# Performance work log

Hardware: AMD Instinct MI355X
Metric: run time of the kernel (lower is better)

The kernel has to match this reference:

```python
import jax, jax.numpy as jnp
import numpy as np

TOP_K = 32

def setup_inputs() -> dict:
    key = jax.random.key(0)
    x = jax.random.normal(key, (4096, 32768), dtype=jnp.float32)
    return {"x": x}

def reference(x) -> jnp.ndarray:
    bsz, d_sae = x.shape
    k = min(TOP_K, d_sae)
    # top-k indices per row (unsorted order does not matter for masking)
    _, idxs = jax.lax.top_k(x, k)  # [batch, k]
    rows = jnp.arange(bsz)[:, None]  # [batch, 1]
    mask = jnp.zeros_like(x).at[rows, idxs].set(1.0)
    return mask * x
```

## Files before the change

kernel.cpp:

```cpp
#include <hip/hip_runtime.h>

#define TOPK    32
#define ROW     32768
#define THREADS 512
#define WAVES   8
#define VPT     16
#define BINS    2048
#define CAP     2048

__device__ __forceinline__ unsigned int f2key(float f) {
    unsigned int u = __float_as_uint(f);
    return u ^ (0x80000000u | (unsigned int)((int)u >> 31));
}
__device__ __forceinline__ float key2f(unsigned int k) {
    unsigned int u = (k & 0x80000000u) ? (k & 0x7fffffffu) : ~k;
    return __uint_as_float(u);
}

struct Shared {
    unsigned int hist[BINS];
    unsigned int wsum[WAVES];
    unsigned int sel_g, sel_gabove;
    unsigned int sel_bin, sel_above;
    unsigned int cand_cnt;
    unsigned int cnt_s;
    float        cf[CAP];
    unsigned int cidx[CAP];
};

__device__ __forceinline__ void hist_select(Shared& sh, int t, int lane,
                                            int wave, unsigned int kk) {
    const int base = wave * 256 + lane * 4;
    unsigned int h0 = sh.hist[base + 0], h1 = sh.hist[base + 1];
    unsigned int h2 = sh.hist[base + 2], h3 = sh.hist[base + 3];
    unsigned int p = h0 + h1 + h2 + h3;
    unsigned int s = p;
#pragma unroll
    for (int off = 1; off < 64; off <<= 1) {
        unsigned int vv = __shfl_down(s, off);
        if (lane + off < 64) s += vv;
    }
    if (lane == 0) sh.wsum[wave] = s;
    __syncthreads();

    if (t == 0) {
        unsigned int above = 0; int g = WAVES - 1;
        for (int w = WAVES - 1; w >= 0; --w) {
            if (above + sh.wsum[w] >= kk) { g = w; break; }
            above += sh.wsum[w];
        }
        sh.sel_g = (unsigned int)g; sh.sel_gabove = above;
    }
    __syncthreads();

    if (wave == (int)sh.sel_g) {
        unsigned int a = sh.sel_gabove + (s - p);
        unsigned int hh[4] = {h0, h1, h2, h3};
#pragma unroll
        for (int j = 3; j >= 0; --j) {
            unsigned int h = hh[j];
            if (a < kk && a + h >= kk) {
                sh.sel_bin = (unsigned int)(base + j);
                sh.sel_above = a;
            }
            a += h;
        }
    }
    __syncthreads();
}

__global__ __launch_bounds__(THREADS, 4) void topk_scatter_kernel(
    const float* __restrict__ x, float* __restrict__ out) {

    __shared__ Shared sh;
    const int row  = blockIdx.x;
    const int t    = threadIdx.x;
    const int lane = t & 63;
    const int wave = t >> 6;

    const float4* __restrict__ xin =
        reinterpret_cast<const float4*>(x + (size_t)row * ROW);
    float* __restrict__ orow = out + (size_t)row * ROW;

    float4 v[VPT];
#pragma unroll
    for (int i = 0; i < VPT; ++i) v[i] = xin[i * THREADS + t];

#pragma unroll
    for (int b = 0; b < 4; ++b) sh.hist[t + b * THREADS] = 0;
    if (t == 0) sh.cand_cnt = 0;
    __syncthreads();

    float m = -__builtin_inff();
#pragma unroll
    for (int i = 0; i < VPT; ++i)
        m = fmaxf(m, fmaxf(fmaxf(v[i].x, v[i].y), fmaxf(v[i].z, v[i].w)));

    atomicAdd(&sh.hist[f2key(m) >> 21], 1u);
    __syncthreads();

    hist_select(sh, t, lane, wave, TOPK);

    const float L = key2f(sh.sel_bin << 21);

#pragma unroll
    for (int i = 0; i < VPT; ++i) {
#pragma unroll
        for (int j = 0; j < 4; ++j) {
            float f = (&v[i].x)[j];
            if (f >= L) {
                unsigned int pos = atomicAdd(&sh.cand_cnt, 1u);
                if (pos < CAP) {
                    sh.cf[pos]   = f;
                    sh.cidx[pos] = (unsigned int)((i * THREADS + t) * 4 + j);
                }
            }
        }
    }
    __syncthreads();
    const unsigned int C = sh.cand_cnt;

    if (C <= CAP) {
        for (unsigned int i = t; i < C; i += THREADS) {
            float ki = sh.cf[i]; unsigned int ii = sh.cidx[i];
            unsigned int r = 0;
            for (unsigned int j = 0; j < C; ++j) {
                float kj = sh.cf[j];
                unsigned int ij = sh.cidx[j];
                r += (kj > ki || (kj == ki && ij < ii)) ? 1u : 0u;
            }
            if (r < TOPK) orow[ii] = ki;
        }
        return;
    }

    unsigned int prefix = 0; int pbits = 0;
    unsigned int kk = TOPK, e = 0;
    for (int r = 0; r < 3; ++r) {
        const int shift = (r == 0) ? 21 : (r == 1 ? 10 : 0);
        const int bits  = (r == 2) ? 10 : 11;
        const unsigned int msk = (1u << bits) - 1u;
        __syncthreads();
#pragma unroll
        for (int b = 0; b < 4; ++b) sh.hist[t + b * THREADS] = 0;
        __syncthreads();
#pragma unroll
        for (int i = 0; i < VPT; ++i) {
#pragma unroll
            for (int j = 0; j < 4; ++j) {
                unsigned int key = f2key((&v[i].x)[j]);
                bool match = (pbits == 0) || ((key >> (32 - pbits)) == prefix);
                if (match) atomicAdd(&sh.hist[(key >> shift) & msk], 1u);
            }
        }
        __syncthreads();
        hist_select(sh, t, lane, wave, kk);
        kk = kk - sh.sel_above;
        e  = sh.hist[sh.sel_bin];
        prefix = (prefix << bits) | sh.sel_bin;
        pbits += bits;
    }
    const unsigned int T = prefix;

    unsigned int Cc = ROW;
    if (e != kk) {
        unsigned int lo = 0, hi = ROW;
        while (hi - lo > 1u) {
            unsigned int mid = (lo + hi) >> 1;
            __syncthreads();
            if (t == 0) sh.cnt_s = 0;
            __syncthreads();
            unsigned int c = 0;
#pragma unroll
            for (int i = 0; i < VPT; ++i) {
#pragma unroll
                for (int j = 0; j < 4; ++j) {
                    unsigned int key = f2key((&v[i].x)[j]);
                    unsigned int idx = (unsigned int)((i * THREADS + t) * 4 + j);
                    if (key == T && idx < mid) ++c;
                }
            }
            if (c) atomicAdd(&sh.cnt_s, c);
            __syncthreads();
            if (sh.cnt_s >= kk) hi = mid; else lo = mid;
        }
        Cc = hi;
    }

#pragma unroll
    for (int i = 0; i < VPT; ++i) {
#pragma unroll
        for (int j = 0; j < 4; ++j) {
            float f = (&v[i].x)[j];
            unsigned int key = f2key(f);
            unsigned int idx = (unsigned int)((i * THREADS + t) * 4 + j);
            if (key > T || (key == T && idx < Cc)) orow[idx] = f;
        }
    }
}

extern "C" void kernel_launch(void* const* d_in, const int* in_sizes, int n_in,
                              void* d_out, int out_size, void* d_ws, size_t ws_size,
                              hipStream_t stream) {
    const float* x = (const float*)d_in[0];
    float* out = (float*)d_out;
    const int rows = in_sizes[0] / ROW;
    hipMemsetAsync(out, 0, (size_t)out_size * sizeof(float), stream);
    topk_scatter_kernel<<<rows, THREADS, 0, stream>>>(x, out);
}
```

Before: 239.4 us.

## Replace memset plus scatter with two-pass dense write, drop register row cache

Removes the separate hipMemsetAsync and instead writes the full output row densely inside the kernel. During the candidate pass every element at or above the threshold is written and everything else is zeroed, then rejected candidates are cleared afterwards. The block shrinks to 256 threads and no longer holds the row in registers; it re-reads x from global memory (likely L2 hits) on each pass, which should allow higher occupancy. The risk is the extra reads of x, plus a serial single-thread bin scan on the rare fallback path.

New measurement: 340.7 us. 1.42x slower.

```diff
diff --git a/kernel.cpp b/kernel.cpp
--- a/kernel.cpp
+++ b/kernel.cpp
@@ -2,11 +2,11 @@
 
 #define TOPK    32
 #define ROW     32768
-#define THREADS 512
-#define WAVES   8
-#define VPT     16
+#define THREADS 256
+#define WAVES   4
+#define F4PT    32
 #define BINS    2048
-#define CAP     2048
+#define CAP     1024
 
 __device__ __forceinline__ unsigned int f2key(float f) {
     unsigned int u = __float_as_uint(f);
@@ -30,10 +30,11 @@
 
 __device__ __forceinline__ void hist_select(Shared& sh, int t, int lane,
                                             int wave, unsigned int kk) {
-    const int base = wave * 256 + lane * 4;
-    unsigned int h0 = sh.hist[base + 0], h1 = sh.hist[base + 1];
-    unsigned int h2 = sh.hist[base + 2], h3 = sh.hist[base + 3];
-    unsigned int p = h0 + h1 + h2 + h3;
+    const int base = wave * 512 + lane * 8;
+    unsigned int h[8];
+    unsigned int p = 0;
+#pragma unroll
+    for (int j = 0; j < 8; ++j) { h[j] = sh.hist[base + j]; p += h[j]; }
     unsigned int s = p;
 #pragma unroll
     for (int off = 1; off < 64; off <<= 1) {
@@ -55,21 +56,20 @@
 
     if (wave == (int)sh.sel_g) {
         unsigned int a = sh.sel_gabove + (s - p);
-        unsigned int hh[4] = {h0, h1, h2, h3};
-#pragma unroll
-        for (int j = 3; j >= 0; --j) {
-            unsigned int h = hh[j];
-            if (a < kk && a + h >= kk) {
+#pragma unroll
+        for (int j = 7; j >= 0; --j) {
+            unsigned int hh = h[j];
+            if (a < kk && a + hh >= kk) {
                 sh.sel_bin = (unsigned int)(base + j);
                 sh.sel_above = a;
             }
-            a += h;
-        }
-    }
-    __syncthreads();
-}
-
-__global__ __launch_bounds__(THREADS, 4) void topk_scatter_kernel(
+            a += hh;
+        }
+    }
+    __syncthreads();
+}
+
+__global__ __launch_bounds__(THREADS, 8) void topk_twopass_kernel(
     const float* __restrict__ x, float* __restrict__ out) {
 
     __shared__ Shared sh;
@@ -80,22 +80,21 @@
 
     const float4* __restrict__ xin =
         reinterpret_cast<const float4*>(x + (size_t)row * ROW);
+    float4* __restrict__ xout =
+        reinterpret_cast<float4*>(out + (size_t)row * ROW);
     float* __restrict__ orow = out + (size_t)row * ROW;
 
-    float4 v[VPT];
-#pragma unroll
-    for (int i = 0; i < VPT; ++i) v[i] = xin[i * THREADS + t];
-
-#pragma unroll
-    for (int b = 0; b < 4; ++b) sh.hist[t + b * THREADS] = 0;
+#pragma unroll
+    for (int b = 0; b < BINS / THREADS; ++b) sh.hist[t + b * THREADS] = 0;
     if (t == 0) sh.cand_cnt = 0;
     __syncthreads();
 
     float m = -__builtin_inff();
-#pragma unroll
-    for (int i = 0; i < VPT; ++i)
-        m = fmaxf(m, fmaxf(fmaxf(v[i].x, v[i].y), fmaxf(v[i].z, v[i].w)));
-
+#pragma unroll 8
+    for (int i = 0; i < F4PT; ++i) {
+        float4 v = xin[i * THREADS + t];
+        m = fmaxf(m, fmaxf(fmaxf(v.x, v.y), fmaxf(v.z, v.w)));
+    }
     atomicAdd(&sh.hist[f2key(m) >> 21], 1u);
     __syncthreads();
 
@@ -103,12 +102,16 @@
 
     const float L = key2f(sh.sel_bin << 21);
 
-#pragma unroll
-    for (int i = 0; i < VPT; ++i) {
+#pragma unroll 4
+    for (int i = 0; i < F4PT; ++i) {
+        float4 v = xin[i * THREADS + t];
+        float4 o;
 #pragma unroll
         for (int j = 0; j < 4; ++j) {
-            float f = (&v[i].x)[j];
-            if (f >= L) {
+            float f = (&v.x)[j];
+            bool cand = (f >= L);
+            (&o.x)[j] = cand ? f : 0.0f;
+            if (cand) {
                 unsigned int pos = atomicAdd(&sh.cand_cnt, 1u);
                 if (pos < CAP) {
                     sh.cf[pos]   = f;
@@ -116,6 +119,7 @@
                 }
             }
         }
+        xout[i * THREADS + t] = o;
     }
     __syncthreads();
     const unsigned int C = sh.cand_cnt;
@@ -129,7 +133,7 @@
                 unsigned int ij = sh.cidx[j];
                 r += (kj > ki || (kj == ki && ij < ii)) ? 1u : 0u;
             }
-            if (r < TOPK) orow[ii] = ki;
+            if (r >= TOPK) orow[ii] = 0.0f;
         }
         return;
     }
@@ -140,21 +144,30 @@
         const int shift = (r == 0) ? 21 : (r == 1 ? 10 : 0);
         const int bits  = (r == 2) ? 10 : 11;
         const unsigned int msk = (1u << bits) - 1u;
-        __syncthreads();
-#pragma unroll
-        for (int b = 0; b < 4; ++b) sh.hist[t + b * THREADS] = 0;
-        __syncthreads();
-#pragma unroll
-        for (int i = 0; i < VPT; ++i) {
+        const int nb = 1 << bits;
+        __syncthreads();
+        for (int b = t; b < nb; b += THREADS) sh.hist[b] = 0;
+        __syncthreads();
+        for (int i = 0; i < F4PT; ++i) {
+            float4 v = xin[i * THREADS + t];
 #pragma unroll
             for (int j = 0; j < 4; ++j) {
-                unsigned int key = f2key((&v[i].x)[j]);
+                unsigned int key = f2key((&v.x)[j]);
                 bool match = (pbits == 0) || ((key >> (32 - pbits)) == prefix);
                 if (match) atomicAdd(&sh.hist[(key >> shift) & msk], 1u);
             }
         }
         __syncthreads();
-        hist_select(sh, t, lane, wave, kk);
+        if (t == 0) {
+            unsigned int above = 0;
+            for (int b = nb - 1; b >= 0; --b) {
+                unsigned int h = sh.hist[b];
+                if (above + h >= kk) { sh.sel_bin = (unsigned int)b;
+                                       sh.sel_above = above; break; }
+                above += h;
+            }
+        }
+        __syncthreads();
         kk = kk - sh.sel_above;
         e  = sh.hist[sh.sel_bin];
         prefix = (prefix << bits) | sh.sel_bin;
@@ -171,11 +184,11 @@
             if (t == 0) sh.cnt_s = 0;
             __syncthreads();
             unsigned int c = 0;
-#pragma unroll
-            for (int i = 0; i < VPT; ++i) {
+            for (int i = 0; i < F4PT; ++i) {
+                float4 v = xin[i * THREADS + t];
 #pragma unroll
                 for (int j = 0; j < 4; ++j) {
-                    unsigned int key = f2key((&v[i].x)[j]);
+                    unsigned int key = f2key((&v.x)[j]);
                     unsigned int idx = (unsigned int)((i * THREADS + t) * 4 + j);
                     if (key == T && idx < mid) ++c;
                 }
@@ -187,15 +200,17 @@
         Cc = hi;
     }
 
-#pragma unroll
-    for (int i = 0; i < VPT; ++i) {
+    for (int i = 0; i < F4PT; ++i) {
+        float4 v = xin[i * THREADS + t];
+        float4 o;
 #pragma unroll
         for (int j = 0; j < 4; ++j) {
-            float f = (&v[i].x)[j];
+            float f = (&v.x)[j];
             unsigned int key = f2key(f);
             unsigned int idx = (unsigned int)((i * THREADS + t) * 4 + j);
-            if (key > T || (key == T && idx < Cc)) orow[idx] = f;
-        }
+            (&o.x)[j] = (key > T || (key == T && idx < Cc)) ? f : 0.0f;
+        }
+        xout[i * THREADS + t] = o;
     }
 }
 
@@ -205,6 +220,5 @@
     const float* x = (const float*)d_in[0];
     float* out = (float*)d_out;
     const int rows = in_sizes[0] / ROW;
-    hipMemsetAsync(out, 0, (size_t)out_size * sizeof(float), stream);
-    topk_scatter_kernel<<<rows, THREADS, 0, stream>>>(x, out);
-}
+    topk_twopass_kernel<<<rows, THREADS, 0, stream>>>(x, out);
+}
```

## Fuse output zeroing into the top-k kernel and relax LDS barriers

Applied to the files above, without the earlier changes.

Drops the separate hipMemsetAsync. Each block now writes zeros to its own output row while loading that row, then scatters the selected top-k values after a barrier. The fallback radix path writes full float4 rows with masked values instead of scattered scalar stores. Most __syncthreads calls become a raw lgkmcnt wait plus s_barrier, and the candidate capacity is halved to cut LDS use. This saves a launch and a separate pass over the output, but it relies on the zero stores becoming visible before the later scattered stores, and halving CAP sends more rows to the slower radix path.

Result: faster. 224.9 us (-6.1%).

```diff
diff --git a/kernel.cpp b/kernel.cpp
--- a/kernel.cpp
+++ b/kernel.cpp
@@ -6,7 +6,7 @@
 #define WAVES   8
 #define VPT     16
 #define BINS    2048
-#define CAP     2048
+#define CAP     1024
 
 __device__ __forceinline__ unsigned int f2key(float f) {
     unsigned int u = __float_as_uint(f);
@@ -15,6 +15,11 @@
 __device__ __forceinline__ float key2f(unsigned int k) {
     unsigned int u = (k & 0x80000000u) ? (k & 0x7fffffffu) : ~k;
     return __uint_as_float(u);
+}
+
+__device__ __forceinline__ void bar_lds() {
+    asm volatile("s_waitcnt lgkmcnt(0)" ::: "memory");
+    __builtin_amdgcn_s_barrier();
 }
 
 struct Shared {
@@ -41,7 +46,7 @@
         if (lane + off < 64) s += vv;
     }
     if (lane == 0) sh.wsum[wave] = s;
-    __syncthreads();
+    bar_lds();
 
     if (t == 0) {
         unsigned int above = 0; int g = WAVES - 1;
@@ -51,7 +56,7 @@
         }
         sh.sel_g = (unsigned int)g; sh.sel_gabove = above;
     }
-    __syncthreads();
+    bar_lds();
 
     if (wave == (int)sh.sel_g) {
         unsigned int a = sh.sel_gabove + (s - p);
@@ -66,10 +71,10 @@
             a += h;
         }
     }
-    __syncthreads();
-}
-
-__global__ __launch_bounds__(THREADS, 4) void topk_scatter_kernel(
+    bar_lds();
+}
+
+__global__ __launch_bounds__(THREADS, 4) void topk_eager_kernel(
     const float* __restrict__ x, float* __restrict__ out) {
 
     __shared__ Shared sh;
@@ -80,24 +85,31 @@
 
     const float4* __restrict__ xin =
         reinterpret_cast<const float4*>(x + (size_t)row * ROW);
+    float4* __restrict__ xout =
+        reinterpret_cast<float4*>(out + (size_t)row * ROW);
     float* __restrict__ orow = out + (size_t)row * ROW;
 
     float4 v[VPT];
-#pragma unroll
-    for (int i = 0; i < VPT; ++i) v[i] = xin[i * THREADS + t];
-
-#pragma unroll
-    for (int b = 0; b < 4; ++b) sh.hist[t + b * THREADS] = 0;
+    const float4 z4 = make_float4(0.f, 0.f, 0.f, 0.f);
+#pragma unroll
+    for (int i = 0; i < VPT; ++i) {
+        v[i] = xin[i * THREADS + t];
+        xout[i * THREADS + t] = z4;
+    }
+    __builtin_amdgcn_sched_barrier(0);
+
+#pragma unroll
+    for (int b = 0; b < BINS / THREADS; ++b) sh.hist[t + b * THREADS] = 0;
     if (t == 0) sh.cand_cnt = 0;
-    __syncthreads();
 
     float m = -__builtin_inff();
 #pragma unroll
     for (int i = 0; i < VPT; ++i)
         m = fmaxf(m, fmaxf(fmaxf(v[i].x, v[i].y), fmaxf(v[i].z, v[i].w)));
 
+    bar_lds();
     atomicAdd(&sh.hist[f2key(m) >> 21], 1u);
-    __syncthreads();
+    bar_lds();
 
     hist_select(sh, t, lane, wave, TOPK);
 
@@ -117,10 +129,13 @@
             }
         }
     }
-    __syncthreads();
+    bar_lds();
     const unsigned int C = sh.cand_cnt;
 
     if (C <= CAP) {
+        float        wv[2];
+        unsigned int wi[2];
+        int nw = 0;
         for (unsigned int i = t; i < C; i += THREADS) {
             float ki = sh.cf[i]; unsigned int ii = sh.cidx[i];
             unsigned int r = 0;
@@ -129,8 +144,10 @@
                 unsigned int ij = sh.cidx[j];
                 r += (kj > ki || (kj == ki && ij < ii)) ? 1u : 0u;
             }
-            if (r < TOPK) orow[ii] = ki;
-        }
+            if (r < TOPK) { wv[nw] = ki; wi[nw] = ii; ++nw; }
+        }
+        __syncthreads();
+        for (int q = 0; q < nw; ++q) orow[wi[q]] = wv[q];
         return;
     }
 
@@ -140,10 +157,10 @@
         const int shift = (r == 0) ? 21 : (r == 1 ? 10 : 0);
         const int bits  = (r == 2) ? 10 : 11;
         const unsigned int msk = (1u << bits) - 1u;
-        __syncthreads();
-#pragma unroll
-        for (int b = 0; b < 4; ++b) sh.hist[t + b * THREADS] = 0;
-        __syncthreads();
+        bar_lds();
+#pragma unroll
+        for (int b = 0; b < BINS / THREADS; ++b) sh.hist[t + b * THREADS] = 0;
+        bar_lds();
 #pragma unroll
         for (int i = 0; i < VPT; ++i) {
 #pragma unroll
@@ -153,7 +170,7 @@
                 if (match) atomicAdd(&sh.hist[(key >> shift) & msk], 1u);
             }
         }
-        __syncthreads();
+        bar_lds();
         hist_select(sh, t, lane, wave, kk);
         kk = kk - sh.sel_above;
         e  = sh.hist[sh.sel_bin];
@@ -167,9 +184,9 @@
         unsigned int lo = 0, hi = ROW;
         while (hi - lo > 1u) {
             unsigned int mid = (lo + hi) >> 1;
-            __syncthreads();
+            bar_lds();
             if (t == 0) sh.cnt_s = 0;
-            __syncthreads();
+            bar_lds();
             unsigned int c = 0;
 #pragma unroll
             for (int i = 0; i < VPT; ++i) {
@@ -181,21 +198,24 @@
                 }
             }
             if (c) atomicAdd(&sh.cnt_s, c);
-            __syncthreads();
+            bar_lds();
             if (sh.cnt_s >= kk) hi = mid; else lo = mid;
         }
         Cc = hi;
     }
 
+    __syncthreads();
 #pragma unroll
     for (int i = 0; i < VPT; ++i) {
+        float4 o;
 #pragma unroll
         for (int j = 0; j < 4; ++j) {
             float f = (&v[i].x)[j];
             unsigned int key = f2key(f);
             unsigned int idx = (unsigned int)((i * THREADS + t) * 4 + j);
-            if (key > T || (key == T && idx < Cc)) orow[idx] = f;
-        }
+            (&o.x)[j] = (key > T || (key == T && idx < Cc)) ? f : 0.0f;
+        }
+        xout[i * THREADS + t] = o;
     }
 }
 
@@ -205,6 +225,5 @@
     const float* x = (const float*)d_in[0];
     float* out = (float*)d_out;
     const int rows = in_sizes[0] / ROW;
-    hipMemsetAsync(out, 0, (size_t)out_size * sizeof(float), stream);
-    topk_scatter_kernel<<<rows, THREADS, 0, stream>>>(x, out);
-}
+    topk_eager_kernel<<<rows, THREADS, 0, stream>>>(x, out);
+}
```
